# Kernel tuning notes

Measured on AMD Instinct MI355X. Metric: run time of the kernel, lower is better.

## Reference

```python
import jax, jax.numpy as jnp
import numpy as np
import math

BLOCK = 8
BANDS = 8
FEATURE_DIM = 512


def _dct_matrix(n):
    k = np.arange(n)[:, None].astype(np.float64)
    i = np.arange(n)[None, :].astype(np.float64)
    m = np.sqrt(2.0 / n) * np.cos(np.pi * k * (2 * i + 1) / (2 * n))
    m[0, :] = np.sqrt(1.0 / n)
    return m.astype(np.float32)


def _zigzag_flat(n):
    idx = []
    for s in range(2 * n - 1):
        if s % 2 == 0:
            for i in range(min(s, n - 1), max(-1, s - n), -1):
                j = s - i
                if 0 <= i < n and 0 <= j < n:
                    idx.append(i * n + j)
        else:
            for i in range(max(0, s - n + 1), min(s + 1, n)):
                j = s - i
                if 0 <= i < n and 0 <= j < n:
                    idx.append(i * n + j)
    return np.array(idx, dtype=np.int32)


def setup_inputs() -> dict:
    key = jax.random.key(0)
    k_img, k_w, k_b = jax.random.split(key, 3)
    images = jax.random.uniform(k_img, (32, 3, 1024, 1024), dtype=jnp.float32)
    dct_matrix = jnp.asarray(_dct_matrix(BLOCK))
    zigzag_flat = jnp.asarray(_zigzag_flat(BLOCK))  # [64] flat (row*n+col) indices
    raw_dim = 2 * BANDS  # mean + std per frequency band
    proj_w = jax.random.normal(k_w, (FEATURE_DIM, raw_dim), dtype=jnp.float32) * 0.05
    proj_b = jax.random.normal(k_b, (FEATURE_DIM,), dtype=jnp.float32) * 0.01
    return {"images": images, "dct_matrix": dct_matrix, "zigzag_flat": zigzag_flat,
            "proj_w": proj_w, "proj_b": proj_b}


def reference(images, dct_matrix, zigzag_flat, proj_w, proj_b):
    # --- luminance conversion (Y of YCbCr) ---
    lum = 0.299 * images[:, 0] + 0.587 * images[:, 1] + 0.114 * images[:, 2]  # [B,H,W]
    # scale to [0,255] if input is in [0,1] (data-dependent scalar, jit-safe)
    lum = lum * jnp.where(lum.max() <= 1.0, 255.0, 1.0)

    B, H, W = lum.shape
    n = dct_matrix.shape[0]
    nh, nw = H // n, W // n
    # --- block unfold: [B, nh, nw, n, n] ---
    blocks = lum[:, : nh * n, : nw * n].reshape(B, nh, n, nw, n).transpose(0, 1, 3, 2, 4)
    # --- 2D DCT: D @ block @ D^T ---
    dct = jnp.einsum("ki,bhwij,lj->bhwkl", dct_matrix, blocks, dct_matrix)
    # --- zigzag gather: [B, nh, nw, n*n] in JPEG coefficient order ---
    zz = dct.reshape(B, nh, nw, n * n)[..., zigzag_flat]
    # --- frequency band aggregation: split into equal contiguous bands ---
    band_size = (n * n) // BANDS
    bands = jnp.abs(zz.reshape(B, nh, nw, BANDS, band_size))
    band_mean = bands.mean(axis=(1, 2, 4))                 # [B, BANDS]
    band_std = jnp.std(bands, axis=(1, 2, 4), ddof=1)      # [B, BANDS] (torch unbiased std)
    raw = jnp.concatenate([band_mean, band_std], axis=-1)  # [B, 2*BANDS]
    # --- linear projection to feature_dim ---
    return raw @ proj_w.T + proj_b
```

## Files before the change

kernel.cpp:

```cpp
#include <hip/hip_runtime.h>

#define HW 1024
#define CH_STRIDE (1024*1024)
#define IMG_STRIDE (3*1024*1024)

constexpr float DCM[8][8] = {
    {0.35355339059327376f, 0.35355339059327376f, 0.35355339059327376f, 0.35355339059327376f,
     0.35355339059327376f, 0.35355339059327376f, 0.35355339059327376f, 0.35355339059327376f},
    {0.49039264020161522f, 0.41573480615127262f, 0.27778511650980111f, 0.09754516100806413f,
    -0.09754516100806413f,-0.27778511650980111f,-0.41573480615127262f,-0.49039264020161522f},
    {0.46193976625564337f, 0.19134171618254489f,-0.19134171618254489f,-0.46193976625564337f,
    -0.46193976625564337f,-0.19134171618254489f, 0.19134171618254489f, 0.46193976625564337f},
    {0.41573480615127262f,-0.09754516100806413f,-0.49039264020161522f,-0.27778511650980111f,
     0.27778511650980111f, 0.49039264020161522f, 0.09754516100806413f,-0.41573480615127262f},
    {0.35355339059327376f,-0.35355339059327376f,-0.35355339059327376f, 0.35355339059327376f,
     0.35355339059327376f,-0.35355339059327376f,-0.35355339059327376f, 0.35355339059327376f},
    {0.27778511650980111f,-0.49039264020161522f, 0.09754516100806413f, 0.41573480615127262f,
    -0.41573480615127262f,-0.09754516100806413f, 0.49039264020161522f,-0.27778511650980111f},
    {0.19134171618254489f,-0.46193976625564337f, 0.46193976625564337f,-0.19134171618254489f,
    -0.19134171618254489f, 0.46193976625564337f,-0.46193976625564337f, 0.19134171618254489f},
    {0.09754516100806413f,-0.27778511650980111f, 0.41573480615127262f,-0.49039264020161522f,
     0.49039264020161522f,-0.41573480615127262f, 0.27778511650980111f,-0.09754516100806413f}
};

constexpr int BAND[64] = {
    0,0,0,0,1,1,3,3,
    0,0,0,1,2,3,3,5,
    0,1,1,2,3,3,5,5,
    1,1,2,3,3,5,5,6,
    1,2,2,4,4,5,6,6,
    2,2,4,4,5,6,6,7,
    2,4,4,5,6,7,7,7,
    4,4,6,6,7,7,7,7
};

__device__ __forceinline__ float wave_reduce_add(float v) {
    #pragma unroll
    for (int off = 32; off > 0; off >>= 1)
        v += __shfl_xor(v, off, 64);
    return v;
}

__global__ __launch_bounds__(256) void dct_band_kernel(
    const float* __restrict__ images,
    double* __restrict__ partials,
    float* __restrict__ wgmax)
{
    const int tid = threadIdx.x;
    const int wg = blockIdx.x;
    const int img = wg >> 6;
    const int chunk = wg & 63;
    const int t = chunk * 256 + tid;
    const int by = t >> 7;
    const int bx = t & 127;

    const float* base = images + (size_t)img * IMG_STRIDE + (size_t)(by * 8) * HW + bx * 8;

    float lum[8][8];
    float fmax_v = 0.0f;
    #pragma unroll
    for (int r = 0; r < 8; ++r) {
        const float4* pr = (const float4*)(base + (size_t)r * HW);
        const float4* pg = (const float4*)(base + CH_STRIDE + (size_t)r * HW);
        const float4* pb = (const float4*)(base + 2 * CH_STRIDE + (size_t)r * HW);
        float4 R0 = pr[0], R1 = pr[1];
        float4 G0 = pg[0], G1 = pg[1];
        float4 B0 = pb[0], B1 = pb[1];
        float rr[8] = {R0.x, R0.y, R0.z, R0.w, R1.x, R1.y, R1.z, R1.w};
        float gg[8] = {G0.x, G0.y, G0.z, G0.w, G1.x, G1.y, G1.z, G1.w};
        float bb[8] = {B0.x, B0.y, B0.z, B0.w, B1.x, B1.y, B1.z, B1.w};
        #pragma unroll
        for (int c = 0; c < 8; ++c) {
            float v = 0.299f * rr[c] + 0.587f * gg[c] + 0.114f * bb[c];
            lum[r][c] = v;
            fmax_v = fmaxf(fmax_v, v);
        }
    }

    #pragma unroll
    for (int j = 0; j < 8; ++j) {
        float col[8];
        #pragma unroll
        for (int i = 0; i < 8; ++i) col[i] = lum[i][j];
        #pragma unroll
        for (int k = 0; k < 8; ++k) {
            float s = 0.0f;
            #pragma unroll
            for (int i = 0; i < 8; ++i) s += DCM[k][i] * col[i];
            lum[k][j] = s;
        }
    }

    float sband[8] = {0,0,0,0,0,0,0,0};
    float qband[8] = {0,0,0,0,0,0,0,0};
    #pragma unroll
    for (int k = 0; k < 8; ++k) {
        float row[8];
        #pragma unroll
        for (int j = 0; j < 8; ++j) row[j] = lum[k][j];
        #pragma unroll
        for (int l = 0; l < 8; ++l) {
            float s = 0.0f;
            #pragma unroll
            for (int j = 0; j < 8; ++j) s += row[j] * DCM[l][j];
            float a = fabsf(s);
            const int b = BAND[k * 8 + l];
            sband[b] += a;
            qband[b] += a * a;
        }
    }

    #pragma unroll
    for (int b = 0; b < 8; ++b) {
        sband[b] = wave_reduce_add(sband[b]);
        qband[b] = wave_reduce_add(qband[b]);
    }
    #pragma unroll
    for (int off = 32; off > 0; off >>= 1)
        fmax_v = fmaxf(fmax_v, __shfl_xor(fmax_v, off, 64));

    __shared__ float lds_s[4][8];
    __shared__ float lds_q[4][8];
    __shared__ float lds_m[4];
    const int wave = tid >> 6;
    const int lane = tid & 63;
    if (lane == 0) {
        #pragma unroll
        for (int b = 0; b < 8; ++b) { lds_s[wave][b] = sband[b]; lds_q[wave][b] = qband[b]; }
        lds_m[wave] = fmax_v;
    }
    __syncthreads();
    if (tid < 8) {
        float s = lds_s[0][tid] + lds_s[1][tid] + lds_s[2][tid] + lds_s[3][tid];
        partials[wg * 16 + tid] = (double)s;
    } else if (tid < 16) {
        const int b = tid - 8;
        float q = lds_q[0][b] + lds_q[1][b] + lds_q[2][b] + lds_q[3][b];
        partials[wg * 16 + tid] = (double)q;
    } else if (tid == 16) {
        wgmax[wg] = fmaxf(fmaxf(lds_m[0], lds_m[1]), fmaxf(lds_m[2], lds_m[3]));
    }
}

__global__ __launch_bounds__(256) void finalize_kernel(
    const double* __restrict__ partials,
    const float* __restrict__ wgmax,
    const float* __restrict__ proj_w,
    const float* __restrict__ proj_b,
    float* __restrict__ out)
{
    const int img = blockIdx.x;
    const int tid = threadIdx.x;

    float m = 0.0f;
    #pragma unroll
    for (int k = 0; k < 8; ++k) m = fmaxf(m, wgmax[tid + k * 256]);
    #pragma unroll
    for (int off = 32; off > 0; off >>= 1)
        m = fmaxf(m, __shfl_xor(m, off, 64));
    __shared__ float smax[4];
    if ((tid & 63) == 0) smax[tid >> 6] = m;

    const int s = tid >> 4;
    const int tsub = tid & 15;
    double acc = 0.0;
    #pragma unroll
    for (int k = 0; k < 4; ++k)
        acc += partials[(size_t)(img * 64 + tsub + k * 16) * 16 + s];
    __shared__ double dred[16][17];
    dred[s][tsub] = acc;
    __syncthreads();

    __shared__ float raw[16];
    const float gmax = fmaxf(fmaxf(smax[0], smax[1]), fmaxf(smax[2], smax[3]));
    const float scale = (gmax <= 1.0f) ? 255.0f : 1.0f;

    __shared__ double totals[16];
    if (tid < 16) {
        double tot = 0.0;
        #pragma unroll
        for (int k = 0; k < 16; ++k) tot += dred[tid][k];
        totals[tid] = tot;
    }
    __syncthreads();
    if (tid < 8) {
        const double S1 = totals[tid];
        const double S2 = totals[8 + tid];
        const double N = 131072.0;
        double mean = S1 / N;
        double var = (S2 - S1 * S1 / N) / (N - 1.0);
        if (var < 0.0) var = 0.0;
        raw[tid]     = scale * (float)mean;
        raw[8 + tid] = scale * (float)sqrt(var);
    }
    __syncthreads();

    #pragma unroll
    for (int o = 0; o < 2; ++o) {
        const int f = tid + o * 256;
        float accp = proj_b[f];
        #pragma unroll
        for (int r = 0; r < 16; ++r)
            accp += raw[r] * proj_w[f * 16 + r];
        out[img * 512 + f] = accp;
    }
}

extern "C" void kernel_launch(void* const* d_in, const int* in_sizes, int n_in,
                              void* d_out, int out_size, void* d_ws, size_t ws_size,
                              hipStream_t stream) {
    const float* images = (const float*)d_in[0];
    const float* proj_w = (const float*)d_in[3];
    const float* proj_b = (const float*)d_in[4];
    float* out = (float*)d_out;

    double* partials = (double*)d_ws;
    float* wgmax = (float*)(partials + 2048 * 16);

    dct_band_kernel<<<2048, 256, 0, stream>>>(images, partials, wgmax);
    finalize_kernel<<<32, 256, 0, stream>>>(partials, wgmax, proj_w, proj_b, out);
}
```

Measured before the change: 543.6 us.

## Stage image rows through LDS with double-buffered async global-to-LDS loads

Result: faster. 516.2 us (-5.0%).

```diff
diff --git a/kernel.cpp b/kernel.cpp
--- a/kernel.cpp
+++ b/kernel.cpp
@@ -41,68 +41,101 @@
     return v;
 }
 
+#define GLOAD_LDS16(g, l)                                                              \
+    __builtin_amdgcn_global_load_lds((const __attribute__((address_space(1))) void*)(g), \
+                                     (__attribute__((address_space(3))) void*)(l),       \
+                                     16, 0, 0)
+
+template<int VM>
+__device__ __forceinline__ void wait_vm_barrier() {
+    asm volatile("s_waitcnt vmcnt(%0)\n\ts_barrier" :: "i"(VM) : "memory");
+}
+__device__ __forceinline__ void plain_barrier() {
+    asm volatile("s_waitcnt lgkmcnt(0)\n\ts_barrier" ::: "memory");
+}
+
 __global__ __launch_bounds__(256) void dct_band_kernel(
     const float* __restrict__ images,
     double* __restrict__ partials,
     float* __restrict__ wgmax)
 {
+    __shared__ __align__(16) float smem[2][6 * 1024];
+
     const int tid = threadIdx.x;
     const int wg = blockIdx.x;
     const int img = wg >> 6;
-    const int chunk = wg & 63;
-    const int t = chunk * 256 + tid;
-    const int by = t >> 7;
-    const int bx = t & 127;
-
-    const float* base = images + (size_t)img * IMG_STRIDE + (size_t)(by * 8) * HW + bx * 8;
-
-    float lum[8][8];
+    const int pair = wg & 63;
+    const int row0 = pair * 16;
+    const int h = tid >> 7;
+    const int bx = tid & 127;
+
+    const float* img_base = images + (size_t)img * IMG_STRIDE;
+    const int wave_u = (tid >> 6) * 256;
+
+    float S[8][8];
+    #pragma unroll
+    for (int k = 0; k < 8; ++k)
+        #pragma unroll
+        for (int j = 0; j < 8; ++j) S[k][j] = 0.0f;
     float fmax_v = 0.0f;
-    #pragma unroll
-    for (int r = 0; r < 8; ++r) {
-        const float4* pr = (const float4*)(base + (size_t)r * HW);
-        const float4* pg = (const float4*)(base + CH_STRIDE + (size_t)r * HW);
-        const float4* pb = (const float4*)(base + 2 * CH_STRIDE + (size_t)r * HW);
-        float4 R0 = pr[0], R1 = pr[1];
-        float4 G0 = pg[0], G1 = pg[1];
-        float4 B0 = pb[0], B1 = pb[1];
-        float rr[8] = {R0.x, R0.y, R0.z, R0.w, R1.x, R1.y, R1.z, R1.w};
-        float gg[8] = {G0.x, G0.y, G0.z, G0.w, G1.x, G1.y, G1.z, G1.w};
-        float bb[8] = {B0.x, B0.y, B0.z, B0.w, B1.x, B1.y, B1.z, B1.w};
-        #pragma unroll
-        for (int c = 0; c < 8; ++c) {
-            float v = 0.299f * rr[c] + 0.587f * gg[c] + 0.114f * bb[c];
-            lum[r][c] = v;
+
+    auto issue_chunk = [&](int c, int p) {
+        #pragma unroll
+        for (int ch = 0; ch < 3; ++ch) {
+            #pragma unroll
+            for (int hh = 0; hh < 2; ++hh) {
+                const float* g = img_base + (size_t)ch * CH_STRIDE
+                               + (size_t)(row0 + hh * 8 + c) * HW + tid * 4;
+                float* l = &smem[p][(ch * 2 + hh) * 1024 + wave_u];
+                GLOAD_LDS16(g, l);
+            }
+        }
+    };
+
+    auto fold_chunk = [&](int c, int p) {
+        const int o = bx * 8;
+        float4 r0 = *(const float4*)&smem[p][(0 * 2 + h) * 1024 + o];
+        float4 r1 = *(const float4*)&smem[p][(0 * 2 + h) * 1024 + o + 4];
+        float4 g0 = *(const float4*)&smem[p][(1 * 2 + h) * 1024 + o];
+        float4 g1 = *(const float4*)&smem[p][(1 * 2 + h) * 1024 + o + 4];
+        float4 b0 = *(const float4*)&smem[p][(2 * 2 + h) * 1024 + o];
+        float4 b1 = *(const float4*)&smem[p][(2 * 2 + h) * 1024 + o + 4];
+        float rr[8] = {r0.x, r0.y, r0.z, r0.w, r1.x, r1.y, r1.z, r1.w};
+        float gg[8] = {g0.x, g0.y, g0.z, g0.w, g1.x, g1.y, g1.z, g1.w};
+        float bb[8] = {b0.x, b0.y, b0.z, b0.w, b1.x, b1.y, b1.z, b1.w};
+        float lum[8];
+        #pragma unroll
+        for (int j = 0; j < 8; ++j) {
+            float v = 0.299f * rr[j] + 0.587f * gg[j] + 0.114f * bb[j];
+            lum[j] = v;
             fmax_v = fmaxf(fmax_v, v);
         }
-    }
-
-    #pragma unroll
-    for (int j = 0; j < 8; ++j) {
-        float col[8];
-        #pragma unroll
-        for (int i = 0; i < 8; ++i) col[i] = lum[i][j];
-        #pragma unroll
-        for (int k = 0; k < 8; ++k) {
-            float s = 0.0f;
+        #pragma unroll
+        for (int k = 0; k < 8; ++k)
             #pragma unroll
-            for (int i = 0; i < 8; ++i) s += DCM[k][i] * col[i];
-            lum[k][j] = s;
-        }
-    }
+            for (int j = 0; j < 8; ++j)
+                S[k][j] += DCM[k][c] * lum[j];
+    };
+
+    issue_chunk(0, 0);
+    #define STEP(c, VMW)                                   \
+        plain_barrier();                                   \
+        if ((c) + 1 < 8) issue_chunk((c) + 1, ((c) + 1) & 1); \
+        wait_vm_barrier<VMW>();                            \
+        fold_chunk((c), (c) & 1);
+    STEP(0, 6) STEP(1, 6) STEP(2, 6) STEP(3, 6)
+    STEP(4, 6) STEP(5, 6) STEP(6, 6) STEP(7, 0)
+    #undef STEP
 
     float sband[8] = {0,0,0,0,0,0,0,0};
     float qband[8] = {0,0,0,0,0,0,0,0};
     #pragma unroll
     for (int k = 0; k < 8; ++k) {
-        float row[8];
-        #pragma unroll
-        for (int j = 0; j < 8; ++j) row[j] = lum[k][j];
         #pragma unroll
         for (int l = 0; l < 8; ++l) {
             float s = 0.0f;
             #pragma unroll
-            for (int j = 0; j < 8; ++j) s += row[j] * DCM[l][j];
+            for (int j = 0; j < 8; ++j) s += S[k][j] * DCM[l][j];
             float a = fabsf(s);
             const int b = BAND[k * 8 + l];
             sband[b] += a;
```
